# Performance work log

Hardware: AMD Instinct MI355X
Metric: run time of the kernel (lower is better)

## Reference

```python
import jax, jax.numpy as jnp
import numpy as np

N = 100000
E = 1600000
F_IN = 128
HID = 128
C = 10
NEG_SLOPE = 0.2


def setup_inputs() -> dict:
    key = jax.random.key(0)
    ks = jax.random.split(key, 12)
    x = jax.random.normal(ks[0], (N, F_IN), dtype=jnp.float32)
    edge_index = jax.random.randint(ks[1], (2, E), 0, N, dtype=jnp.int64)
    batch = jnp.zeros((N,), dtype=jnp.int64)
    s1 = 1.0 / np.sqrt(F_IN)
    s2 = 1.0 / np.sqrt(HID)
    return {
        "x": x,
        "edge_index": edge_index,
        "batch": batch,
        "W1": jax.random.normal(ks[2], (F_IN, HID), dtype=jnp.float32) * s1,
        "a_src1": jax.random.normal(ks[3], (HID,), dtype=jnp.float32) * s2,
        "a_dst1": jax.random.normal(ks[4], (HID,), dtype=jnp.float32) * s2,
        "b1": jnp.zeros((HID,), dtype=jnp.float32),
        "W2": jax.random.normal(ks[5], (HID, HID), dtype=jnp.float32) * s2,
        "a_src2": jax.random.normal(ks[6], (HID,), dtype=jnp.float32) * s2,
        "a_dst2": jax.random.normal(ks[7], (HID,), dtype=jnp.float32) * s2,
        "b2": jnp.zeros((HID,), dtype=jnp.float32),
        "Wlin": jax.random.normal(ks[8], (HID, C), dtype=jnp.float32) * s2,
        "blin": jnp.zeros((C,), dtype=jnp.float32),
    }


def gat_conv(x, src, dst, W, a_src, a_dst, b):
    # PyG GATConv, heads=1: h = xW; alpha_e = softmax_dst(leaky_relu(a_src.h[src] + a_dst.h[dst]))
    h = x @ W                                  # [N, H]
    alpha_s = h @ a_src                        # [N]
    alpha_d = h @ a_dst                        # [N]
    e = jax.nn.leaky_relu(alpha_s[src] + alpha_d[dst], NEG_SLOPE)  # [E]
    m = jax.ops.segment_max(e, dst, num_segments=N)                # per-dst max (stable softmax)
    ex = jnp.exp(e - m[dst])
    denom = jax.ops.segment_sum(ex, dst, num_segments=N)
    alpha = ex / (denom[dst] + 1e-16)          # [E]
    out = jax.ops.segment_sum(h[src] * alpha[:, None], dst, num_segments=N)
    return out + b


def reference(x, edge_index, batch, W1, a_src1, a_dst1, b1, W2, a_src2, a_dst2, b2, Wlin, blin):
    x = x.astype(jnp.float32)
    loops = jnp.arange(N, dtype=edge_index.dtype)
    src = jnp.concatenate([edge_index[0], loops])  # add_self_loops=True
    dst = jnp.concatenate([edge_index[1], loops])
    h = jax.nn.relu(gat_conv(x, src, dst, W1, a_src1, a_dst1, b1))
    h = jax.nn.relu(gat_conv(h, src, dst, W2, a_src2, a_dst2, b2))
    # dropout(p=0.5) is identity in eval mode
    return h @ Wlin + blin
```

## Files before the change

### kernel.cpp

```cpp
#include <hip/hip_runtime.h>

#define N_NODES 100000
#define N_EDGES 1600000
#define TOTE    (N_EDGES + N_NODES)
#define NEG     0.2f
#define NB      ((N_NODES + 255) >> 8)
#define BCAP    5120

typedef __attribute__((ext_vector_type(8))) short bf16x8;
typedef __attribute__((ext_vector_type(4))) float floatx4;

__device__ __forceinline__ unsigned short f2bf(float f) {
  unsigned int u = __float_as_uint(f);
  u += 0x7fffu + ((u >> 16) & 1u);
  return (unsigned short)(u >> 16);
}
__device__ __forceinline__ float bf_lo(unsigned int r) { return __uint_as_float(r << 16); }
__device__ __forceinline__ float bf_hi(unsigned int r) { return __uint_as_float(r & 0xffff0000u); }

__global__ __launch_bounds__(256) void k_wprep(const float* __restrict__ W1, const float* __restrict__ W2,
                                               unsigned short* __restrict__ B1hi, unsigned short* __restrict__ B1lo,
                                               unsigned short* __restrict__ B2hi, unsigned short* __restrict__ B2lo,
                                               int* __restrict__ bucketCnt) {
  int b = blockIdx.x;
  int t = threadIdx.x;
  if (b == 16) {
    for (int i = t; i < NB * 16; i += 256) bucketCnt[i] = 0;
    return;
  }
  const float* W = (b < 8) ? W1 : W2;
  unsigned short* Bh = (b < 8) ? B1hi : B2hi;
  unsigned short* Bl = (b < 8) ? B1lo : B2lo;
  int ntile = b & 7;
  int kq = t >> 6, lane = t & 63;
  int q = lane >> 4, m = lane & 15;
  int n = ntile * 16 + m;
  union { unsigned short us[8]; uint4 u4; } hi, lo;
#pragma unroll
  for (int j = 0; j < 8; ++j) {
    int k = kq * 32 + q * 8 + j;
    float w = W[(size_t)k * 128 + n];
    unsigned int u = __float_as_uint(w);
    hi.us[j] = (unsigned short)(u >> 16);
    float res = w - __uint_as_float(u & 0xffff0000u);
    lo.us[j] = f2bf(res);
  }
  size_t fo = ((size_t)(ntile * 4 + kq) * 64 + lane) * 8;
  *reinterpret_cast<uint4*>(Bh + fo) = hi.u4;
  *reinterpret_cast<uint4*>(Bl + fo) = lo.u4;
}

__global__ __launch_bounds__(256) void k_binA(const int* __restrict__ ei, int* __restrict__ bucketCnt,
                                              unsigned int* __restrict__ binned) {
  __shared__ int hist[NB];
  __shared__ int cur[NB];
  int t = threadIdx.x;
  for (int b = t; b < NB; b += 256) hist[b] = 0;
  __syncthreads();
  unsigned int pk[16]; int bk[16];
#pragma unroll
  for (int j = 0; j < 16; ++j) {
    int idx = blockIdx.x * 4096 + j * 256 + t;
    if (idx < N_EDGES) {
      int s = ei[idx], d = ei[N_EDGES + idx];
      bk[j] = d >> 8;
      pk[j] = ((unsigned int)s << 8) | (unsigned int)(d & 255);
      atomicAdd(&hist[bk[j]], 1);
    } else bk[j] = -1;
  }
  __syncthreads();
  for (int b = t; b < NB; b += 256) {
    int h = hist[b];
    if (h) cur[b] = b * BCAP + atomicAdd(&bucketCnt[b * 16], h);
  }
  __syncthreads();
#pragma unroll
  for (int j = 0; j < 16; ++j) {
    if (bk[j] >= 0) {
      int pos = atomicAdd(&cur[bk[j]], 1);
      binned[pos] = pk[j];
    }
  }
}

__global__ __launch_bounds__(512) void k_bin_scan(const int* __restrict__ bucketCnt,
                                                  int* __restrict__ binOffs) {
  __shared__ int sc[512];
  int t = threadIdx.x;
  int v = (t < NB) ? bucketCnt[t * 16] : 0;
  sc[t] = v; __syncthreads();
  for (int off = 1; off < 512; off <<= 1) {
    int x = (t >= off) ? sc[t - off] : 0;
    __syncthreads();
    sc[t] += x;
    __syncthreads();
  }
  int excl = sc[t] - v;
  if (t <= NB) binOffs[t] = excl;
}

__global__ __launch_bounds__(256) void k_binB(const unsigned int* __restrict__ binned,
                                              const int* __restrict__ binOffs,
                                              int* __restrict__ offs, int* __restrict__ srcs) {
  __shared__ int cnt[256];
  __shared__ int sc[256];
  __shared__ int cur[256];
  int b = blockIdx.x;
  int t = threadIdx.x;
  int node0 = b << 8;
  int nNodes = min(256, N_NODES - node0);
  int cntE = binOffs[b + 1] - binOffs[b];
  int e0 = b * BCAP, e1 = e0 + cntE;
  int base = binOffs[b] + node0;

  cnt[t] = 0; __syncthreads();
  for (int i = e0 + t; i < e1; i += 256) atomicAdd(&cnt[binned[i] & 255u], 1);
  __syncthreads();

  int v = (t < nNodes) ? cnt[t] + 1 : 0;
  sc[t] = v; __syncthreads();
  for (int off = 1; off < 256; off <<= 1) {
    int x = (t >= off) ? sc[t - off] : 0;
    __syncthreads();
    sc[t] += x;
    __syncthreads();
  }
  int excl = sc[t] - v;
  if (t < nNodes) {
    offs[node0 + t] = base + excl;
    srcs[base + excl] = node0 + t;
  }
  cur[t] = excl + 1;
  __syncthreads();

  for (int i = e0 + t; i < e1; i += 256) {
    unsigned int e = binned[i];
    int j = (int)(e & 255u);
    int s = (int)(e >> 8);
    int p = atomicAdd(&cur[j], 1);
    srcs[base + p] = s;
  }
  if (b == 0 && t == 0) offs[N_NODES] = TOTE;
}

template <bool SPLIT>
__global__ __launch_bounds__(256) void k_gemm_mfma(const void* __restrict__ Aptr,
                                                   const unsigned short* __restrict__ Bhi,
                                                   const unsigned short* __restrict__ Blo,
                                                   unsigned short* __restrict__ Cb,
                                                   const float* __restrict__ avS, const float* __restrict__ avD,
                                                   float* __restrict__ aS, float* __restrict__ aD,
                                                   float* __restrict__ slotS, float* __restrict__ slotD) {
  __shared__ unsigned short sC[64 * 136];
  __shared__ float redS[64 * 4], redD[64 * 4];
  __shared__ float mS[64], mD[64];
  int t = threadIdx.x;
  int w = t >> 6, lane = t & 63;
  int q = lane >> 4, m = lane & 15;
  int rbase = blockIdx.x * 64;

  floatx4 acc[4][2];
#pragma unroll
  for (int mt = 0; mt < 4; ++mt)
#pragma unroll
    for (int nt = 0; nt < 2; ++nt) acc[mt][nt] = (floatx4){0.f, 0.f, 0.f, 0.f};

#pragma unroll
  for (int k0 = 0; k0 < 4; ++k0) {
    bf16x8 Bh[2], Bl[2], Ah[4], Al[4];
#pragma unroll
    for (int nt = 0; nt < 2; ++nt) {
      int ntg = w * 2 + nt;
      size_t fo = ((size_t)(ntg * 4 + k0) * 64 + lane) * 8;
      Bh[nt] = *reinterpret_cast<const bf16x8*>(Bhi + fo);
      Bl[nt] = *reinterpret_cast<const bf16x8*>(Blo + fo);
    }
#pragma unroll
    for (int mt = 0; mt < 4; ++mt) {
      int row = rbase + mt * 16 + m;
      row = min(row, N_NODES - 1);
      if constexpr (SPLIT) {
        const float* ap = (const float*)Aptr + (size_t)row * 128 + k0 * 32 + q * 8;
        float4 v0 = *reinterpret_cast<const float4*>(ap);
        float4 v1 = *reinterpret_cast<const float4*>(ap + 4);
        float av[8] = {v0.x, v0.y, v0.z, v0.w, v1.x, v1.y, v1.z, v1.w};
        union { unsigned short us[8]; bf16x8 v; } uh, ul;
#pragma unroll
        for (int j = 0; j < 8; ++j) {
          unsigned int u = __float_as_uint(av[j]);
          uh.us[j] = (unsigned short)(u >> 16);
          float res = av[j] - __uint_as_float(u & 0xffff0000u);
          ul.us[j] = f2bf(res);
        }
        Ah[mt] = uh.v; Al[mt] = ul.v;
      } else {
        const unsigned short* ap = (const unsigned short*)Aptr + (size_t)row * 128 + k0 * 32 + q * 8;
        Ah[mt] = *reinterpret_cast<const bf16x8*>(ap);
      }
    }
#pragma unroll
    for (int mt = 0; mt < 4; ++mt)
#pragma unroll
      for (int nt = 0; nt < 2; ++nt) {
        acc[mt][nt] = __builtin_amdgcn_mfma_f32_16x16x32_bf16(Ah[mt], Bh[nt], acc[mt][nt], 0, 0, 0);
        acc[mt][nt] = __builtin_amdgcn_mfma_f32_16x16x32_bf16(Ah[mt], Bl[nt], acc[mt][nt], 0, 0, 0);
        if constexpr (SPLIT)
          acc[mt][nt] = __builtin_amdgcn_mfma_f32_16x16x32_bf16(Al[mt], Bh[nt], acc[mt][nt], 0, 0, 0);
      }
  }

  float avs[2], avd[2];
#pragma unroll
  for (int nt = 0; nt < 2; ++nt) {
    int c = w * 32 + nt * 16 + m;
    avs[nt] = avS[c];
    avd[nt] = avD[c];
  }
#pragma unroll
  for (int mt = 0; mt < 4; ++mt)
#pragma unroll
    for (int r = 0; r < 4; ++r) {
      float ps = acc[mt][0][r] * avs[0] + acc[mt][1][r] * avs[1];
      float pd = acc[mt][0][r] * avd[0] + acc[mt][1][r] * avd[1];
      ps += __shfl_xor(ps, 1); pd += __shfl_xor(pd, 1);
      ps += __shfl_xor(ps, 2); pd += __shfl_xor(pd, 2);
      ps += __shfl_xor(ps, 4); pd += __shfl_xor(pd, 4);
      ps += __shfl_xor(ps, 8); pd += __shfl_xor(pd, 8);
      if (m == 0) {
        int rl = mt * 16 + q * 4 + r;
        redS[rl * 4 + w] = ps;
        redD[rl * 4 + w] = pd;
      }
    }

#pragma unroll
  for (int mt = 0; mt < 4; ++mt)
#pragma unroll
    for (int nt = 0; nt < 2; ++nt)
#pragma unroll
      for (int r = 0; r < 4; ++r) {
        int rl = mt * 16 + q * 4 + r;
        int cl = w * 32 + nt * 16 + m;
        sC[rl * 136 + cl] = f2bf(acc[mt][nt][r]);
      }
  __syncthreads();

#pragma unroll
  for (int i = 0; i < 4; ++i) {
    int idx = i * 256 + t;
    int rl = idx >> 4, kk = idx & 15;
    int gr = rbase + rl;
    if (gr < N_NODES)
      *reinterpret_cast<uint4*>(Cb + (size_t)gr * 128 + kk * 8) =
          *reinterpret_cast<const uint4*>(sC + rl * 136 + kk * 8);
  }

  if (t < 64) {
    int gr = rbase + t;
    bool ok = gr < N_NODES;
    float ps = redS[t * 4] + redS[t * 4 + 1] + redS[t * 4 + 2] + redS[t * 4 + 3];
    float pd = redD[t * 4] + redD[t * 4 + 1] + redD[t * 4 + 2] + redD[t * 4 + 3];
    if (ok) { aS[gr] = ps; aD[gr] = pd; }
    mS[t] = ok ? ps : -1e30f;
    mD[t] = ok ? pd : -1e30f;
  }
  __syncthreads();
#pragma unroll
  for (int off = 32; off > 0; off >>= 1) {
    if (t < off) { mS[t] = fmaxf(mS[t], mS[t + off]); mD[t] = fmaxf(mD[t], mD[t + off]); }
    __syncthreads();
  }
  if (t == 0) { slotS[blockIdx.x] = mS[0]; slotD[blockIdx.x] = mD[0]; }
}

__global__ __launch_bounds__(256) void k_gmax(const float* __restrict__ slotS,
                                              const float* __restrict__ slotD,
                                              int n, float* __restrict__ gMh) {
  __shared__ float sS[256], sD[256];
  int t = threadIdx.x;
  float ms = -1e30f, md = -1e30f;
  for (int i = t; i < n; i += 256) { ms = fmaxf(ms, slotS[i]); md = fmaxf(md, slotD[i]); }
  sS[t] = ms; sD[t] = md;
  __syncthreads();
#pragma unroll
  for (int off = 128; off > 0; off >>= 1) {
    if (t < off) { sS[t] = fmaxf(sS[t], sS[t + off]); sD[t] = fmaxf(sD[t], sD[t + off]); }
    __syncthreads();
  }
  if (t == 0) {
    float M = sS[0] + sD[0];
    gMh[0] = (M > 0.f) ? M : NEG * M;
  }
}

#define FMA8(E, R)                                     \
  do {                                                 \
    acc[0] += (E) * bf_lo((R).x); acc[1] += (E) * bf_hi((R).x); \
    acc[2] += (E) * bf_lo((R).y); acc[3] += (E) * bf_hi((R).y); \
    acc[4] += (E) * bf_lo((R).z); acc[5] += (E) * bf_hi((R).z); \
    acc[6] += (E) * bf_lo((R).w); acc[7] += (E) * bf_hi((R).w); \
  } while (0)

#define LDG(R0, R1, R2, R3, E0, E1, E2, E3, J)                                                   \
  do {                                                                                           \
    float2 q0 = pairs[pbase + (J) + 0];                                                          \
    float2 q1 = pairs[pbase + (J) + 1];                                                          \
    float2 q2 = pairs[pbase + (J) + 2];                                                          \
    float2 q3 = pairs[pbase + (J) + 3];                                                          \
    E0 = q0.x; E1 = q1.x; E2 = q2.x; E3 = q3.x;                                                  \
    R0 = *reinterpret_cast<const uint4*>(hbl + ((size_t)(unsigned)__float_as_int(q0.y) << 7));   \
    R1 = *reinterpret_cast<const uint4*>(hbl + ((size_t)(unsigned)__float_as_int(q1.y) << 7));   \
    R2 = *reinterpret_cast<const uint4*>(hbl + ((size_t)(unsigned)__float_as_int(q2.y) << 7));   \
    R3 = *reinterpret_cast<const uint4*>(hbl + ((size_t)(unsigned)__float_as_int(q3.y) << 7));   \
  } while (0)
#define FMAG(R0, R1, R2, R3, E0, E1, E2, E3) \
  do { FMA8(E0, R0); FMA8(E1, R1); FMA8(E2, R2); FMA8(E3, R3); } while (0)

template <bool FINAL>
__global__ __launch_bounds__(256) void k_aggregate(const unsigned short* __restrict__ hb,
                                                   const float* __restrict__ aS,
                                                   const float* __restrict__ aD,
                                                   const int* __restrict__ offs,
                                                   const int* __restrict__ srcs,
                                                   const float* __restrict__ bias,
                                                   const float* __restrict__ gMh,
                                                   unsigned short* __restrict__ outb,
                                                   const float* __restrict__ Wl,
                                                   const float* __restrict__ bl,
                                                   float* __restrict__ out) {
  __shared__ float2 pairs[16 * 17];
  __shared__ float sWt[FINAL ? 10 * 144 : 1];
  __shared__ float sbl[FINAL ? 16 : 1];
  int t = threadIdx.x;
  if constexpr (FINAL) {
    if (t < 128) {
      int jj = t >> 5, ii = t & 31;
#pragma unroll
      for (int c = 0; c < 10; ++c) sWt[c * 144 + jj * 36 + ii] = Wl[t * 10 + c];
    }
    if (t < 10) sbl[t] = bl[t];
    __syncthreads();
  }
  int g = t >> 4;
  int l = t & 15;
  int dst = blockIdx.x * 16 + g;
  float Mh = gMh[0];
  int beg = offs[dst], end = offs[dst + 1];
  float adn = aD[dst];
  float denom = 0.f;
  float acc[8];
#pragma unroll
  for (int k = 0; k < 8; ++k) acc[k] = 0.f;
  const int pbase = g * 17;
  const unsigned short* hbl = hb + l * 8;

  uint4 ra0, ra1, ra2, ra3, rb0, rb1, rb2, rb3;
  float ea0, ea1, ea2, ea3, eb0, eb1, eb2, eb3;

  for (int chunk = beg; chunk < end; chunk += 16) {
    int i = chunk + l;
    float ex = 0.f; int s = 0;
    if (i < end) {
      s = srcs[i];
      float e = aS[s] + adn;
      e = (e > 0.f) ? e : NEG * e;
      ex = __expf(e - Mh);
    }
    denom += ex;
    pairs[pbase + l] = make_float2(ex, __int_as_float(s));
    int cnt = end - chunk; if (cnt > 16) cnt = 16;
    LDG(ra0, ra1, ra2, ra3, ea0, ea1, ea2, ea3, 0);
    int j = 0;
    for (;;) {
      bool more = (j + 4) < cnt;
      if (more) LDG(rb0, rb1, rb2, rb3, eb0, eb1, eb2, eb3, j + 4);
      FMAG(ra0, ra1, ra2, ra3, ea0, ea1, ea2, ea3);
      j += 4;
      if (!more) break;
      bool more2 = (j + 4) < cnt;
      if (more2) LDG(ra0, ra1, ra2, ra3, ea0, ea1, ea2, ea3, j + 4);
      FMAG(rb0, rb1, rb2, rb3, eb0, eb1, eb2, eb3);
      j += 4;
      if (!more2) break;
    }
  }

  denom += __shfl_xor(denom, 1);
  denom += __shfl_xor(denom, 2);
  denom += __shfl_xor(denom, 4);
  denom += __shfl_xor(denom, 8);
  float inv = 1.f / (denom + 1e-16f);
  float4 b0 = *reinterpret_cast<const float4*>(bias + l * 8);
  float4 b1 = *reinterpret_cast<const float4*>(bias + l * 8 + 4);
  float o0 = fmaxf(acc[0] * inv + b0.x, 0.f), o1 = fmaxf(acc[1] * inv + b0.y, 0.f);
  float o2 = fmaxf(acc[2] * inv + b0.z, 0.f), o3 = fmaxf(acc[3] * inv + b0.w, 0.f);
  float o4 = fmaxf(acc[4] * inv + b1.x, 0.f), o5 = fmaxf(acc[5] * inv + b1.y, 0.f);
  float o6 = fmaxf(acc[6] * inv + b1.z, 0.f), o7 = fmaxf(acc[7] * inv + b1.w, 0.f);

  if constexpr (!FINAL) {
    union { unsigned short us[8]; uint4 u4; } oo;
    oo.us[0] = f2bf(o0); oo.us[1] = f2bf(o1); oo.us[2] = f2bf(o2); oo.us[3] = f2bf(o3);
    oo.us[4] = f2bf(o4); oo.us[5] = f2bf(o5); oo.us[6] = f2bf(o6); oo.us[7] = f2bf(o7);
    *reinterpret_cast<uint4*>(outb + (size_t)dst * 128 + l * 8) = oo.u4;
  } else {
    float p[10];
#pragma unroll
    for (int c = 0; c < 10; ++c) {
      const float4* wp = reinterpret_cast<const float4*>(&sWt[c * 144 + (l >> 2) * 36 + (l & 3) * 8]);
      float4 w0 = wp[0], w1 = wp[1];
      p[c] = o0 * w0.x + o1 * w0.y + o2 * w0.z + o3 * w0.w +
             o4 * w1.x + o5 * w1.y + o6 * w1.z + o7 * w1.w;
    }
#pragma unroll
    for (int c = 0; c < 10; ++c) {
      p[c] += __shfl_xor(p[c], 1);
      p[c] += __shfl_xor(p[c], 2);
      p[c] += __shfl_xor(p[c], 4);
      p[c] += __shfl_xor(p[c], 8);
    }
    if (l == 0) {
      float* orow = out + (size_t)dst * 10;
      *reinterpret_cast<float2*>(orow + 0) = make_float2(p[0] + sbl[0], p[1] + sbl[1]);
      *reinterpret_cast<float2*>(orow + 2) = make_float2(p[2] + sbl[2], p[3] + sbl[3]);
      *reinterpret_cast<float2*>(orow + 4) = make_float2(p[4] + sbl[4], p[5] + sbl[5]);
      *reinterpret_cast<float2*>(orow + 6) = make_float2(p[6] + sbl[6], p[7] + sbl[7]);
      *reinterpret_cast<float2*>(orow + 8) = make_float2(p[8] + sbl[8], p[9] + sbl[9]);
    }
  }
}

extern "C" void kernel_launch(void* const* d_in, const int* in_sizes, int n_in,
                              void* d_out, int out_size, void* d_ws, size_t ws_size,
                              hipStream_t stream) {
  const float* x   = (const float*)d_in[0];
  const int*   ei  = (const int*)d_in[1];
  const float* W1  = (const float*)d_in[3];
  const float* as1 = (const float*)d_in[4];
  const float* ad1 = (const float*)d_in[5];
  const float* b1  = (const float*)d_in[6];
  const float* W2  = (const float*)d_in[7];
  const float* as2 = (const float*)d_in[8];
  const float* ad2 = (const float*)d_in[9];
  const float* b2  = (const float*)d_in[10];
  const float* Wl  = (const float*)d_in[11];
  const float* bl  = (const float*)d_in[12];
  float* out = (float*)d_out;

  char* p = (char*)d_ws;
  unsigned short* hb   = (unsigned short*)p; p += (size_t)N_NODES * 128 * sizeof(unsigned short);
  unsigned short* hagg = (unsigned short*)p; p += (size_t)N_NODES * 128 * sizeof(unsigned short);
  float* aS    = (float*)p; p += (size_t)N_NODES * sizeof(float);
  float* aD    = (float*)p; p += (size_t)N_NODES * sizeof(float);
  int* offs    = (int*)p;   p += (size_t)(N_NODES + 4) * sizeof(int);
  int* srcs    = (int*)p;   p += (size_t)TOTE * sizeof(int);
  int* bucketCnt = (int*)p; p += (size_t)NB * 16 * sizeof(int);
  int* binOffs   = (int*)p; p += (size_t)(NB + 4) * sizeof(int);
  float* slotS = (float*)p; p += 2048 * sizeof(float);
  float* slotD = (float*)p; p += 2048 * sizeof(float);
  float* gMh = (float*)p;   p += 4 * sizeof(float);
  unsigned short* B1hi = (unsigned short*)p; p += 128 * 128 * sizeof(unsigned short);
  unsigned short* B1lo = (unsigned short*)p; p += 128 * 128 * sizeof(unsigned short);
  unsigned short* B2hi = (unsigned short*)p; p += 128 * 128 * sizeof(unsigned short);
  unsigned short* B2lo = (unsigned short*)p; p += 128 * 128 * sizeof(unsigned short);
  unsigned int* binned = (unsigned int*)hagg;

  int binBlocks = (N_EDGES + 4095) / 4096;

  k_wprep<<<17, 256, 0, stream>>>(W1, W2, B1hi, B1lo, B2hi, B2lo, bucketCnt);
  k_binA<<<binBlocks, 256, 0, stream>>>(ei, bucketCnt, binned);
  k_bin_scan<<<1, 512, 0, stream>>>(bucketCnt, binOffs);
  k_binB<<<NB, 256, 0, stream>>>(binned, binOffs, offs, srcs);

  int gemmBlocks = (N_NODES + 63) / 64;
  int aggBlocks  = N_NODES / 16;

  k_gemm_mfma<true><<<gemmBlocks, 256, 0, stream>>>(x, B1hi, B1lo, hb, as1, ad1, aS, aD, slotS, slotD);
  k_gmax<<<1, 256, 0, stream>>>(slotS, slotD, gemmBlocks, gMh);
  k_aggregate<false><<<aggBlocks, 256, 0, stream>>>(hb, aS, aD, offs, srcs, b1, gMh, hagg,
                                                    nullptr, nullptr, nullptr);
  k_gemm_mfma<false><<<gemmBlocks, 256, 0, stream>>>(hagg, B2hi, B2lo, hb, as2, ad2, aS, aD, slotS, slotD);
  k_gmax<<<1, 256, 0, stream>>>(slotS, slotD, gemmBlocks, gMh);
  k_aggregate<true><<<aggBlocks, 256, 0, stream>>>(hb, aS, aD, offs, srcs, b2, gMh, hagg,
                                                   Wl, bl, out);
}
```

Measured before the change: 353.1 us.

## Stage GEMM A tile into LDS via direct global-to-LDS loads

```diff
diff --git a/kernel.cpp b/kernel.cpp
--- a/kernel.cpp
+++ b/kernel.cpp
@@ -144,26 +144,44 @@
 }
 
 template <bool SPLIT>
-__global__ __launch_bounds__(256) void k_gemm_mfma(const void* __restrict__ Aptr,
+__global__ __launch_bounds__(256, 4) void k_gemm_mfma(const void* __restrict__ Aptr,
                                                    const unsigned short* __restrict__ Bhi,
                                                    const unsigned short* __restrict__ Blo,
                                                    unsigned short* __restrict__ Cb,
                                                    const float* __restrict__ avS, const float* __restrict__ avD,
                                                    float* __restrict__ aS, float* __restrict__ aD,
                                                    float* __restrict__ slotS, float* __restrict__ slotD) {
-  __shared__ unsigned short sC[64 * 136];
+  constexpr int SRCB  = SPLIT ? 512 : 256;
+  constexpr int ROWB  = SPLIT ? 528 : 272;
+  constexpr int ABYTES = 64 * ROWB;
+  constexpr int CHUNKS = ABYTES / 1024;
+  __shared__ char sbuf[ABYTES];
   __shared__ float redS[64 * 4], redD[64 * 4];
   __shared__ float mS[64], mD[64];
   int t = threadIdx.x;
   int w = t >> 6, lane = t & 63;
   int q = lane >> 4, m = lane & 15;
   int rbase = blockIdx.x * 64;
+  const char* Ab = (const char*)Aptr;
+
+  for (int c = w; c < CHUNKS; c += 4) {
+    int L = c * 1024 + lane * 16;
+    int r = L / ROWB;
+    int off = L - r * ROWB;
+    int gr = min(rbase + r, N_NODES - 1);
+    const char* src = (off < SRCB) ? (Ab + (size_t)gr * SRCB + off) : Ab;
+    __builtin_amdgcn_global_load_lds((const __attribute__((address_space(1))) void*)src,
+                                     (__attribute__((address_space(3))) void*)(sbuf + c * 1024),
+                                     16, 0, 0);
+  }
 
   floatx4 acc[4][2];
 #pragma unroll
   for (int mt = 0; mt < 4; ++mt)
 #pragma unroll
     for (int nt = 0; nt < 2; ++nt) acc[mt][nt] = (floatx4){0.f, 0.f, 0.f, 0.f};
+
+  __syncthreads();
 
 #pragma unroll
   for (int k0 = 0; k0 < 4; ++k0) {
@@ -177,12 +195,11 @@
     }
 #pragma unroll
     for (int mt = 0; mt < 4; ++mt) {
-      int row = rbase + mt * 16 + m;
-      row = min(row, N_NODES - 1);
+      int R = mt * 16 + m;
       if constexpr (SPLIT) {
-        const float* ap = (const float*)Aptr + (size_t)row * 128 + k0 * 32 + q * 8;
+        const char* ap = sbuf + R * ROWB + k0 * 128 + q * 32;
         float4 v0 = *reinterpret_cast<const float4*>(ap);
-        float4 v1 = *reinterpret_cast<const float4*>(ap + 4);
+        float4 v1 = *reinterpret_cast<const float4*>(ap + 16);
         float av[8] = {v0.x, v0.y, v0.z, v0.w, v1.x, v1.y, v1.z, v1.w};
         union { unsigned short us[8]; bf16x8 v; } uh, ul;
 #pragma unroll
@@ -194,8 +211,7 @@
         }
         Ah[mt] = uh.v; Al[mt] = ul.v;
       } else {
-        const unsigned short* ap = (const unsigned short*)Aptr + (size_t)row * 128 + k0 * 32 + q * 8;
-        Ah[mt] = *reinterpret_cast<const bf16x8*>(ap);
+        Ah[mt] = *reinterpret_cast<const bf16x8*>(sbuf + R * ROWB + k0 * 64 + q * 16);
       }
     }
 #pragma unroll
@@ -232,6 +248,9 @@
         redD[rl * 4 + w] = pd;
       }
     }
+
+  __syncthreads();
+  unsigned short* sC = (unsigned short*)sbuf;
 
 #pragma unroll
   for (int mt = 0; mt < 4; ++mt)
```

New measurement: 333.3 us. 5.6% less time.
